# Kernel optimization log

Hardware: AMD Instinct MI355X
Metric: run time of the kernel (lower is better)

Reference implementation:

```python
import jax, jax.numpy as jnp
import numpy as np

IN_CH = 256
QK_CH = IN_CH // 8  # 32

def setup_inputs() -> dict:
    key = jax.random.key(0)
    ks = jax.random.split(key, 7)
    x = jax.random.normal(ks[0], (4, IN_CH, 64, 64), dtype=jnp.float32)
    s_in = 1.0 / np.sqrt(IN_CH)
    # 1x1 conv weights stored as [out_ch, in_ch]; biases [out_ch]
    Wq = jax.random.uniform(ks[1], (QK_CH, IN_CH), jnp.float32, -s_in, s_in)
    bq = jax.random.uniform(ks[2], (QK_CH,), jnp.float32, -s_in, s_in)
    Wk = jax.random.uniform(ks[3], (QK_CH, IN_CH), jnp.float32, -s_in, s_in)
    bk = jax.random.uniform(ks[4], (QK_CH,), jnp.float32, -s_in, s_in)
    Wv = jax.random.uniform(ks[5], (IN_CH, IN_CH), jnp.float32, -s_in, s_in)
    bv = jax.random.uniform(ks[6], (IN_CH,), jnp.float32, -s_in, s_in)
    return {"x": x, "Wq": Wq, "bq": bq, "Wk": Wk, "bk": bk, "Wv": Wv, "bv": bv}

def reference(x, Wq, bq, Wk, bk, Wv, bv):
    n, c, h, w = x.shape
    xf = x.reshape(n, c, h * w)  # [n, c, hw]
    # 1x1 convs == per-position channel matmuls
    q = jnp.einsum('oc,ncs->nos', Wq, xf) + bq[None, :, None]  # [n, c/8, hw]
    k = jnp.einsum('oc,ncs->nos', Wk, xf) + bk[None, :, None]  # [n, c/8, hw]
    v = jnp.einsum('oc,ncs->nos', Wv, xf) + bv[None, :, None]  # [n, c,  hw]
    # energy[n, i, j] = <q[:, i], k[:, j]>  (no scaling, as in original)
    energy = jnp.einsum('nci,ncj->nij', q, k)  # [n, hw, hw]
    attention = jax.nn.softmax(energy, axis=-1)
    # out[n, c, i] = sum_j v[n, c, j] * attention[n, i, j]
    out = jnp.einsum('ncj,nij->nci', v, attention)
    return out.reshape(n, c, h, w)
```

## Files before the change

### kernel.cpp

```cpp
#include <hip/hip_runtime.h>
#include <hip/hip_bf16.h>
#include <stdint.h>
#include <stddef.h>

typedef unsigned short u16;
typedef unsigned int   u32;
typedef __attribute__((ext_vector_type(8))) short bf16x8;
typedef __attribute__((ext_vector_type(4))) float f32x4;

#define LOG2E   1.44269504f
#define EXP_OFF 23.0831206f

static __device__ __forceinline__ float bf2f(u16 v) {
    u32 u = ((u32)v) << 16; float f; __builtin_memcpy(&f, &u, 4); return f;
}
static __device__ __forceinline__ u16 f2bf(float f) {
    u32 u; __builtin_memcpy(&u, &f, 4);
    u32 r = (u + 0x7fffu + ((u >> 16) & 1u)) >> 16; return (u16)r;
}
static __device__ __forceinline__ float as_f(u32 u) { float f; __builtin_memcpy(&f, &u, 4); return f; }
static __device__ __forceinline__ u32   as_u(float f) { u32 u; __builtin_memcpy(&u, &f, 4); return u; }

static __device__ __forceinline__ int detect_f32_wave0(const void* x, int t) {
    const u32* xw = (const u32*)x;
    int bad = 0;
    #pragma unroll
    for (int k = 0; k < 4; ++k) {
        u32 wv = xw[(t << 2) + k];
        int e = (wv >> 7) & 0xff;
        bad += (e >= 160);
    }
    unsigned long long m = __ballot(bad > 0);
    return (__popcll(m) >= 8) ? 1 : 0;
}


__global__ __launch_bounds__(256) void qkv_proj_mfma(
    const void* __restrict__ x,
    const void* __restrict__ Wq, const void* __restrict__ bq,
    const void* __restrict__ Wk, const void* __restrict__ bk,
    const void* __restrict__ Wv, const void* __restrict__ bv,
    u16* __restrict__ qws, u16* __restrict__ kws, u16* __restrict__ vws,
    int n_off, int nshiftp)
{
    __shared__ u16 Wl[64 * 256];
    __shared__ int dtf;

    const int t    = threadIdx.x;
    const int bid  = blockIdx.x;
    const int n_w  = bid & ((1 << nshiftp) - 1);
    const int rest = bid >> nshiftp;
    const int g    = rest % 5;
    const int it   = rest / 5;
    const int n_g  = n_off + n_w;
    const int i0   = it << 6;

    if (t < 64) { int f = detect_f32_wave0(x, t); if (t == 0) dtf = f; }
    __syncthreads();
    const bool isf32 = (dtf != 0);

    #pragma unroll
    for (int k = 0; k < 16; ++k) {
        int idx  = t + (k << 8);
        int row  = idx >> 6;
        int col4 = (idx & 63) << 2;
        const void* src; int srow;
        if (g == 0) {
            if (row < 32) { src = Wq; srow = row; }
            else          { src = Wk; srow = row - 32; }
        } else { src = Wv; srow = ((g - 1) << 6) + row; }
        ushort4 h;
        if (isf32) {
            float4 wv = *((const float4*)((const float*)src + srow * 256 + col4));
            h.x = f2bf(wv.x); h.y = f2bf(wv.y); h.z = f2bf(wv.z); h.w = f2bf(wv.w);
        } else {
            h = *((const ushort4*)((const u16*)src + srow * 256 + col4));
        }
        *(ushort4*)&Wl[(row << 8) + (col4 ^ ((row & 7) << 3))] = h;
    }
    __syncthreads();

    const int lane = t & 63;
    const int w    = t >> 6;
    const int n16  = lane & 15;
    const int quad = lane >> 4;
    const int i_b  = i0 + (w << 4);
    const int i    = i_b + n16;
    const int swz  = (n16 & 7) << 3;

    f32x4 acc[4];
    #pragma unroll
    for (int f = 0; f < 4; ++f) acc[f] = (f32x4){0.f, 0.f, 0.f, 0.f};

    if (isf32) {
        const float* xp = (const float*)x
            + (((size_t)(n_g * 256 + (quad << 3))) << 12) + i;
        float af[8];
        #pragma unroll
        for (int e = 0; e < 8; ++e) af[e] = xp[(size_t)e << 12];
        #pragma unroll
        for (int c8 = 0; c8 < 8; ++c8) {
            bf16x8 a;
            #pragma unroll
            for (int e = 0; e < 8; ++e) a[e] = (short)f2bf(af[e]);
            if (c8 < 7) {
                const float* xn = xp + (((size_t)(c8 + 1) << 5) << 12);
                #pragma unroll
                for (int e = 0; e < 8; ++e) af[e] = xn[(size_t)e << 12];
            }
            const int c0 = c8 << 5;
            #pragma unroll
            for (int f = 0; f < 4; ++f) {
                const int brow = (f << 4) + n16;
                bf16x8 b = *(const bf16x8*)
                    &Wl[(brow << 8) + ((c0 + (quad << 3)) ^ swz)];
                acc[f] = __builtin_amdgcn_mfma_f32_16x16x32_bf16(a, b, acc[f], 0, 0, 0);
            }
        }
    } else {
        const u16* xp = (const u16*)x
            + (((size_t)(n_g * 256 + (quad << 3))) << 12) + i;
        u16 af[8];
        #pragma unroll
        for (int e = 0; e < 8; ++e) af[e] = xp[(size_t)e << 12];
        #pragma unroll
        for (int c8 = 0; c8 < 8; ++c8) {
            bf16x8 a;
            #pragma unroll
            for (int e = 0; e < 8; ++e) a[e] = (short)af[e];
            if (c8 < 7) {
                const u16* xn = xp + (((size_t)(c8 + 1) << 5) << 12);
                #pragma unroll
                for (int e = 0; e < 8; ++e) af[e] = xn[(size_t)e << 12];
            }
            const int c0 = c8 << 5;
            #pragma unroll
            for (int f = 0; f < 4; ++f) {
                const int brow = (f << 4) + n16;
                bf16x8 b = *(const bf16x8*)
                    &Wl[(brow << 8) + ((c0 + (quad << 3)) ^ swz)];
                acc[f] = __builtin_amdgcn_mfma_f32_16x16x32_bf16(a, b, acc[f], 0, 0, 0);
            }
        }
    }

    if (g == 0) {
        #pragma unroll
        for (int f = 0; f < 4; ++f) {
            const int ol   = (f << 4) + n16;
            const bool isq = (ol < 32);
            const int och  = isq ? ol : (ol - 32);
            float bias;
            if (isf32) bias = ((const float*)(isq ? bq : bk))[och];
            else       bias = bf2f(((const u16*)(isq ? bq : bk))[och]);
            u16* dst = (isq ? qws : kws) + (((size_t)n_w) << 17) + och;
            const float scale = isq ? LOG2E : 1.0f;
            #pragma unroll
            for (int r = 0; r < 4; ++r) {
                const int ii = i_b + (quad << 2) + r;
                dst[(size_t)ii << 5] = f2bf((acc[f][r] + bias) * scale);
            }
        }
    } else {
        #pragma unroll
        for (int f = 0; f < 4; ++f) {
            const int c = ((g - 1) << 6) + (f << 4) + n16;
            float bias = isf32 ? ((const float*)bv)[c]
                               : bf2f(((const u16*)bv)[c]);
            const int i4 = i_b + (quad << 2);
            ushort4 h;
            h.x = f2bf(acc[f][0] + bias);
            h.y = f2bf(acc[f][1] + bias);
            h.z = f2bf(acc[f][2] + bias);
            h.w = f2bf(acc[f][3] + bias);
            const size_t addr = ((size_t)n_w << 20)
                + ((size_t)(c >> 4) << 16)
                + ((size_t)(i4 >> 5) << 9)
                + (size_t)((((((i4 & 31) >> 3) << 4) + (c & 15)) << 3) + (i4 & 7));
            *(ushort4*)(vws + addr) = h;
        }
    }
}

__global__ __launch_bounds__(1024) void flash_mfma9(
    const u16* __restrict__ qws, const u16* __restrict__ kws,
    const u16* __restrict__ vws, void* __restrict__ out,
    const void* __restrict__ x, int n_off, int nshift)
{
    __shared__ __align__(16) char arena[17920];
    __shared__ __align__(16) float lS[64];
    __shared__ int dtf;
    u16*   PsA  = (u16*)arena;
    float* Dbuf = (float*)arena;

    const int t    = threadIdx.x;
    const int lane = t & 63;
    const int w    = t >> 6;
    const int n16  = lane & 15;
    const int quad = lane >> 4;
    const int bid  = blockIdx.x;
    const int n_w  = bid & ((1 << nshift) - 1);
    const int qt   = bid >> nshift;
    const int n_g  = n_off + n_w;
    const int i0   = qt << 6;

    if (t < 64) {
        int f = detect_f32_wave0(x, t);
        if (t == 0) dtf = f;
        lS[t] = 0.f;
    }

    const u16* qb = qws + (((size_t)n_w) << 17);
    const u16* kb = kws + (((size_t)n_w) << 17);
    const u16* vb = vws + (((size_t)n_w) << 20);

    const int qsub_s = w & 3;
    const int jsub   = w >> 2;
    const int cq = w & 7;
    const int jq = w >> 3;

    const bf16x8 qfrag =
        *(const bf16x8*)(qb + ((size_t)(i0 + (qsub_s << 4) + n16) << 5) + (quad << 3));

    f32x4 acc[4][2];
    #pragma unroll
    for (int a = 0; a < 4; ++a)
        #pragma unroll
        for (int b = 0; b < 2; ++b) acc[a][b] = (f32x4){0.f, 0.f, 0.f, 0.f};
    float lp[4] = {0.f, 0.f, 0.f, 0.f};

    const int jcol = (jsub << 4) + n16;
    const int j8   = jcol >> 3;
    const int jlo  = jcol & 7;
    const int ksw  = (jq << 2) + quad;

    const u16* kp = kb + ((size_t)((jsub << 4) + n16) << 5) + (quad << 3);
    const u16* vfp0 = vb + ((size_t)(cq << 1) << 16) + ((size_t)jq << 9)
                         + ((size_t)((quad << 4) + n16) << 3);
    const u16* vfp1 = vfp0 + 65536;

    bf16x8 kcur, knext, vf0, vf1;

    kcur = *(const bf16x8*)(kp);
    {
        u16* Ps = PsA;
        const f32x4 z = {0.f, 0.f, 0.f, 0.f};
        f32x4 s = __builtin_amdgcn_mfma_f32_16x16x32_bf16(qfrag, kcur, z, 0, 0, 0);
        #pragma unroll
        for (int r = 0; r < 4; ++r) {
            const int qrow = (qsub_s << 4) + (quad << 2) + r;
            float p = exp2f(s[r] - EXP_OFF);
            u32 u = as_u(p) & 0xffff0000u;
            lp[r] += as_f(u);
            Ps[qrow * 64 + ((j8 ^ (qrow & 7)) << 3) + jlo] = (u16)(u >> 16);
        }
        knext = *(const bf16x8*)(kp + 2048);
        vf0 = *(const bf16x8*)(vfp0);
        vf1 = *(const bf16x8*)(vfp1);
    }
    __syncthreads();

    for (int tile = 1; tile < 64; ++tile) {
        const int par  = tile & 1;
        u16* Psc = PsA + (par << 12);
        u16* Psp = PsA + ((par ^ 1) << 12);

        kcur = knext;
        if (tile < 63) {
            knext = *(const bf16x8*)(kp + ((size_t)(tile + 1) << 11));
        }

        bf16x8 pa[4];
        #pragma unroll
        for (int qs = 0; qs < 4; ++qs) {
            const int qrow = (qs << 4) + n16;
            pa[qs] = *(const bf16x8*)&Psp[qrow * 64 + ((ksw ^ (qrow & 7)) << 3)];
        }
        #pragma unroll
        for (int qs = 0; qs < 4; ++qs) {
            acc[qs][0] = __builtin_amdgcn_mfma_f32_16x16x32_bf16(pa[qs], vf0, acc[qs][0], 0, 0, 0);
            acc[qs][1] = __builtin_amdgcn_mfma_f32_16x16x32_bf16(pa[qs], vf1, acc[qs][1], 0, 0, 0);
        }

        vf0 = *(const bf16x8*)(vfp0 + ((size_t)tile << 10));
        vf1 = *(const bf16x8*)(vfp1 + ((size_t)tile << 10));

        const f32x4 z = {0.f, 0.f, 0.f, 0.f};
        f32x4 s = __builtin_amdgcn_mfma_f32_16x16x32_bf16(qfrag, kcur, z, 0, 0, 0);
        #pragma unroll
        for (int r = 0; r < 4; ++r) {
            const int qrow = (qsub_s << 4) + (quad << 2) + r;
            float p = exp2f(s[r] - EXP_OFF);
            u32 u = as_u(p) & 0xffff0000u;
            lp[r] += as_f(u);
            Psc[qrow * 64 + ((j8 ^ (qrow & 7)) << 3) + jlo] = (u16)(u >> 16);
        }

        __syncthreads();
    }

    {
        u16* Psp = PsA + (1 << 12);
        bf16x8 pa[4];
        #pragma unroll
        for (int qs = 0; qs < 4; ++qs) {
            const int qrow = (qs << 4) + n16;
            pa[qs] = *(const bf16x8*)&Psp[qrow * 64 + ((ksw ^ (qrow & 7)) << 3)];
        }
        #pragma unroll
        for (int qs = 0; qs < 4; ++qs) {
            acc[qs][0] = __builtin_amdgcn_mfma_f32_16x16x32_bf16(pa[qs], vf0, acc[qs][0], 0, 0, 0);
            acc[qs][1] = __builtin_amdgcn_mfma_f32_16x16x32_bf16(pa[qs], vf1, acc[qs][1], 0, 0, 0);
        }
    }

    #pragma unroll
    for (int r = 0; r < 4; ++r) {
        lp[r] += __shfl_xor(lp[r], 1);
        lp[r] += __shfl_xor(lp[r], 2);
        lp[r] += __shfl_xor(lp[r], 4);
        lp[r] += __shfl_xor(lp[r], 8);
    }
    if (n16 == 0) {
        #pragma unroll
        for (int r = 0; r < 4; ++r)
            atomicAdd(&lS[(qsub_s << 4) + (quad << 2) + r], lp[r]);
    }
    __syncthreads();
    if (t < 64) lS[t] = 1.0f / lS[t];
    const bool isf32 = (dtf != 0);

    for (int chunk = 0; chunk < 4; ++chunk) {
        __syncthreads();
        if (jq == 1 && (cq >> 1) == chunk) {
            #pragma unroll
            for (int qs = 0; qs < 4; ++qs)
                #pragma unroll
                for (int cs = 0; cs < 2; ++cs)
                    *(f32x4*)&Dbuf[(((cq & 1) << 5) + (cs << 4) + n16) * 68 +
                                   (qs << 4) + (quad << 2)] = acc[qs][cs];
        }
        __syncthreads();
        if (jq == 0 && (cq >> 1) == chunk) {
            #pragma unroll
            for (int qs = 0; qs < 4; ++qs)
                #pragma unroll
                for (int cs = 0; cs < 2; ++cs) {
                    float* p = &Dbuf[(((cq & 1) << 5) + (cs << 4) + n16) * 68 +
                                     (qs << 4) + (quad << 2)];
                    f32x4 d = *(f32x4*)p;
                    d += acc[qs][cs];
                    *(f32x4*)p = d;
                }
        }
        __syncthreads();
        const int c_l = t >> 4;
        const int qg  = (t & 15) << 2;
        float4 d  = *(float4*)&Dbuf[c_l * 68 + qg];
        float4 rl = *(float4*)&lS[qg];
        const int c_glob = (chunk << 6) + c_l;
        const size_t ob = (((size_t)(n_g * 256 + c_glob)) << 12) + i0 + qg;
        if (isf32) {
            float4 o = make_float4(d.x * rl.x, d.y * rl.y, d.z * rl.z, d.w * rl.w);
            *(float4*)((float*)out + ob) = o;
        } else {
            union { uint2 v; u16 h[4]; } o;
            o.h[0] = f2bf(d.x * rl.x);
            o.h[1] = f2bf(d.y * rl.y);
            o.h[2] = f2bf(d.z * rl.z);
            o.h[3] = f2bf(d.w * rl.w);
            *(uint2*)((u16*)out + ob) = o.v;
        }
    }
}

extern "C" void kernel_launch(void* const* d_in, const int* in_sizes, int n_in,
                              void* d_out, int out_size, void* d_ws, size_t ws_size,
                              hipStream_t stream)
{
    const void* x  = d_in[0];
    const void* Wq = d_in[1];
    const void* bq = d_in[2];
    const void* Wk = d_in[3];
    const void* bk = d_in[4];
    const void* Wv = d_in[5];
    const void* bv = d_in[6];

    const size_t full_need = (size_t)(4u * 4096u) * (32 + 32 + 256) * 2;
    if (ws_size >= full_need) {
        u16* qws = (u16*)d_ws;
        u16* kws = qws + (size_t)4 * 4096 * 32;
        u16* vws = kws + (size_t)4 * 4096 * 32;
        qkv_proj_mfma<<<dim3(1280), dim3(256), 0, stream>>>(
            x, Wq, bq, Wk, bk, Wv, bv, qws, kws, vws, 0, 2);
        flash_mfma9<<<dim3(256), dim3(1024), 0, stream>>>(
            qws, kws, vws, d_out, x, 0, 2);
    } else {
        u16* qws = (u16*)d_ws;
        u16* kws = qws + (size_t)4096 * 32;
        u16* vws = kws + (size_t)4096 * 32;
        for (int n = 0; n < 4; ++n) {
            qkv_proj_mfma<<<dim3(320), dim3(256), 0, stream>>>(
                x, Wq, bq, Wk, bk, Wv, bv, qws, kws, vws, n, 0);
            flash_mfma9<<<dim3(64), dim3(1024), 0, stream>>>(
                qws, kws, vws, d_out, x, n, 0);
        }
    }
}
```

Baseline: 144.3 us.

## Process two key tiles per barrier with four-buffer P staging

```diff
diff --git a/kernel.cpp b/kernel.cpp
--- a/kernel.cpp
+++ b/kernel.cpp
@@ -182,15 +182,51 @@
     }
 }
 
-__global__ __launch_bounds__(1024) void flash_mfma9(
+static __device__ __forceinline__ void s_tile16(
+    const bf16x8 qfrag, const bf16x8 kc, char* __restrict__ PsW,
+    float* __restrict__ lp, const int* __restrict__ pwoff)
+{
+    const f32x4 zoff = {-EXP_OFF, -EXP_OFF, -EXP_OFF, -EXP_OFF};
+    f32x4 s = __builtin_amdgcn_mfma_f32_16x16x32_bf16(qfrag, kc, zoff, 0, 0, 0);
+    #pragma unroll
+    for (int r = 0; r < 4; ++r) {
+        float p = exp2f(s[r]);
+        u32 u = as_u(p) & 0xffff0000u;
+        lp[r] += as_f(u);
+        *(u16*)(PsW + pwoff[r]) = (u16)(u >> 16);
+    }
+}
+
+static __device__ __forceinline__ void pa_load(
+    const char* __restrict__ PsR, const int* __restrict__ paoff, bf16x8* pa)
+{
+    #pragma unroll
+    for (int qs = 0; qs < 4; ++qs)
+        pa[qs] = *(const bf16x8*)(PsR + paoff[qs]);
+}
+
+static __device__ __forceinline__ void pv_tile16(
+    const bf16x8* pa, const bf16x8 v0, const bf16x8 v1, f32x4 acc[4][2])
+{
+    #pragma unroll
+    for (int qs = 0; qs < 4; ++qs) {
+        acc[qs][0] = __builtin_amdgcn_mfma_f32_16x16x32_bf16(pa[qs], v0, acc[qs][0], 0, 0, 0);
+        acc[qs][1] = __builtin_amdgcn_mfma_f32_16x16x32_bf16(pa[qs], v1, acc[qs][1], 0, 0, 0);
+    }
+}
+
+__global__ __launch_bounds__(1024) void flash_mfma13(
     const u16* __restrict__ qws, const u16* __restrict__ kws,
     const u16* __restrict__ vws, void* __restrict__ out,
     const void* __restrict__ x, int n_off, int nshift)
 {
-    __shared__ __align__(16) char arena[17920];
+    __shared__ __align__(16) char arena[32768];
     __shared__ __align__(16) float lS[64];
     __shared__ int dtf;
-    u16*   PsA  = (u16*)arena;
+    char* buf0 = arena;
+    char* buf1 = arena + 8192;
+    char* buf2 = arena + 16384;
+    char* buf3 = arena + 24576;
     float* Dbuf = (float*)arena;
 
     const int t    = threadIdx.x;
@@ -234,84 +270,101 @@
     const int jlo  = jcol & 7;
     const int ksw  = (jq << 2) + quad;
 
+    int pwoff[4];
+    #pragma unroll
+    for (int r = 0; r < 4; ++r) {
+        const int qrow = (qsub_s << 4) + (quad << 2) + r;
+        pwoff[r] = (qrow * 64 + ((j8 ^ (qrow & 7)) << 3) + jlo) << 1;
+    }
+    int paoff[4];
+    #pragma unroll
+    for (int qs = 0; qs < 4; ++qs) {
+        const int qrow = (qs << 4) + n16;
+        paoff[qs] = (qrow * 64 + ((ksw ^ (qrow & 7)) << 3)) << 1;
+    }
+
     const u16* kp = kb + ((size_t)((jsub << 4) + n16) << 5) + (quad << 3);
     const u16* vfp0 = vb + ((size_t)(cq << 1) << 16) + ((size_t)jq << 9)
                          + ((size_t)((quad << 4) + n16) << 3);
     const u16* vfp1 = vfp0 + 65536;
 
-    bf16x8 kcur, knext, vf0, vf1;
-
-    kcur = *(const bf16x8*)(kp);
+    bf16x8 kc0, kc1, kn0, kn1;
+    bf16x8 vA0, vA1, vA2, vA3;
+    bf16x8 vB0, vB1, vB2, vB3;
+    bf16x8 pa[4];
+
+    kc0 = *(const bf16x8*)(kp);
+    kc1 = *(const bf16x8*)(kp + 2048);
+    s_tile16(qfrag, kc0, buf0, lp, pwoff);
+    s_tile16(qfrag, kc1, buf1, lp, pwoff);
+    kn0 = *(const bf16x8*)(kp + 2 * 2048);
+    kn1 = *(const bf16x8*)(kp + 3 * 2048);
+    vA0 = *(const bf16x8*)(vfp0);
+    vA1 = *(const bf16x8*)(vfp1);
+    vA2 = *(const bf16x8*)(vfp0 + 1024);
+    vA3 = *(const bf16x8*)(vfp1 + 1024);
+    __syncthreads();
+
+    const u16* kpp  = kp + 4 * 2048;
+    const u16* vpp0 = vfp0 + 2 * 1024;
+    const u16* vpp1 = vfp1 + 2 * 1024;
+
+    for (int pr = 0; pr < 15; ++pr) {
+        kc0 = kn0; kc1 = kn1;
+        kn0 = *(const bf16x8*)(kpp);
+        kn1 = *(const bf16x8*)(kpp + 2048);
+        kpp += 4096;
+        pa_load(buf0, paoff, pa);
+        s_tile16(qfrag, kc0, buf2, lp, pwoff);
+        pv_tile16(pa, vA0, vA1, acc);
+        pa_load(buf1, paoff, pa);
+        s_tile16(qfrag, kc1, buf3, lp, pwoff);
+        pv_tile16(pa, vA2, vA3, acc);
+        vB0 = *(const bf16x8*)(vpp0);
+        vB1 = *(const bf16x8*)(vpp1);
+        vB2 = *(const bf16x8*)(vpp0 + 1024);
+        vB3 = *(const bf16x8*)(vpp1 + 1024);
+        vpp0 += 2048; vpp1 += 2048;
+        __syncthreads();
+
+        kc0 = kn0; kc1 = kn1;
+        kn0 = *(const bf16x8*)(kpp);
+        kn1 = *(const bf16x8*)(kpp + 2048);
+        kpp += 4096;
+        pa_load(buf2, paoff, pa);
+        s_tile16(qfrag, kc0, buf0, lp, pwoff);
+        pv_tile16(pa, vB0, vB1, acc);
+        pa_load(buf3, paoff, pa);
+        s_tile16(qfrag, kc1, buf1, lp, pwoff);
+        pv_tile16(pa, vB2, vB3, acc);
+        vA0 = *(const bf16x8*)(vpp0);
+        vA1 = *(const bf16x8*)(vpp1);
+        vA2 = *(const bf16x8*)(vpp0 + 1024);
+        vA3 = *(const bf16x8*)(vpp1 + 1024);
+        vpp0 += 2048; vpp1 += 2048;
+        __syncthreads();
+    }
+
     {
-        u16* Ps = PsA;
-        const f32x4 z = {0.f, 0.f, 0.f, 0.f};
-        f32x4 s = __builtin_amdgcn_mfma_f32_16x16x32_bf16(qfrag, kcur, z, 0, 0, 0);
-        #pragma unroll
-        for (int r = 0; r < 4; ++r) {
-            const int qrow = (qsub_s << 4) + (quad << 2) + r;
-            float p = exp2f(s[r] - EXP_OFF);
-            u32 u = as_u(p) & 0xffff0000u;
-            lp[r] += as_f(u);
-            Ps[qrow * 64 + ((j8 ^ (qrow & 7)) << 3) + jlo] = (u16)(u >> 16);
-        }
-        knext = *(const bf16x8*)(kp + 2048);
-        vf0 = *(const bf16x8*)(vfp0);
-        vf1 = *(const bf16x8*)(vfp1);
-    }
-    __syncthreads();
-
-    for (int tile = 1; tile < 64; ++tile) {
-        const int par  = tile & 1;
-        u16* Psc = PsA + (par << 12);
-        u16* Psp = PsA + ((par ^ 1) << 12);
-
-        kcur = knext;
-        if (tile < 63) {
-            knext = *(const bf16x8*)(kp + ((size_t)(tile + 1) << 11));
-        }
-
-        bf16x8 pa[4];
-        #pragma unroll
-        for (int qs = 0; qs < 4; ++qs) {
-            const int qrow = (qs << 4) + n16;
-            pa[qs] = *(const bf16x8*)&Psp[qrow * 64 + ((ksw ^ (qrow & 7)) << 3)];
-        }
-        #pragma unroll
-        for (int qs = 0; qs < 4; ++qs) {
-            acc[qs][0] = __builtin_amdgcn_mfma_f32_16x16x32_bf16(pa[qs], vf0, acc[qs][0], 0, 0, 0);
-            acc[qs][1] = __builtin_amdgcn_mfma_f32_16x16x32_bf16(pa[qs], vf1, acc[qs][1], 0, 0, 0);
-        }
-
-        vf0 = *(const bf16x8*)(vfp0 + ((size_t)tile << 10));
-        vf1 = *(const bf16x8*)(vfp1 + ((size_t)tile << 10));
-
-        const f32x4 z = {0.f, 0.f, 0.f, 0.f};
-        f32x4 s = __builtin_amdgcn_mfma_f32_16x16x32_bf16(qfrag, kcur, z, 0, 0, 0);
-        #pragma unroll
-        for (int r = 0; r < 4; ++r) {
-            const int qrow = (qsub_s << 4) + (quad << 2) + r;
-            float p = exp2f(s[r] - EXP_OFF);
-            u32 u = as_u(p) & 0xffff0000u;
-            lp[r] += as_f(u);
-            Psc[qrow * 64 + ((j8 ^ (qrow & 7)) << 3) + jlo] = (u16)(u >> 16);
-        }
-
+        kc0 = kn0; kc1 = kn1;
+        pa_load(buf0, paoff, pa);
+        s_tile16(qfrag, kc0, buf2, lp, pwoff);
+        pv_tile16(pa, vA0, vA1, acc);
+        pa_load(buf1, paoff, pa);
+        s_tile16(qfrag, kc1, buf3, lp, pwoff);
+        pv_tile16(pa, vA2, vA3, acc);
+        vB0 = *(const bf16x8*)(vpp0);
+        vB1 = *(const bf16x8*)(vpp1);
+        vB2 = *(const bf16x8*)(vpp0 + 1024);
+        vB3 = *(const bf16x8*)(vpp1 + 1024);
         __syncthreads();
     }
 
     {
-        u16* Psp = PsA + (1 << 12);
-        bf16x8 pa[4];
-        #pragma unroll
-        for (int qs = 0; qs < 4; ++qs) {
-            const int qrow = (qs << 4) + n16;
-            pa[qs] = *(const bf16x8*)&Psp[qrow * 64 + ((ksw ^ (qrow & 7)) << 3)];
-        }
-        #pragma unroll
-        for (int qs = 0; qs < 4; ++qs) {
-            acc[qs][0] = __builtin_amdgcn_mfma_f32_16x16x32_bf16(pa[qs], vf0, acc[qs][0], 0, 0, 0);
-            acc[qs][1] = __builtin_amdgcn_mfma_f32_16x16x32_bf16(pa[qs], vf1, acc[qs][1], 0, 0, 0);
-        }
+        pa_load(buf2, paoff, pa);
+        pv_tile16(pa, vB0, vB1, acc);
+        pa_load(buf3, paoff, pa);
+        pv_tile16(pa, vB2, vB3, acc);
     }
 
     #pragma unroll
@@ -393,7 +446,7 @@
         u16* vws = kws + (size_t)4 * 4096 * 32;
         qkv_proj_mfma<<<dim3(1280), dim3(256), 0, stream>>>(
             x, Wq, bq, Wk, bk, Wv, bv, qws, kws, vws, 0, 2);
-        flash_mfma9<<<dim3(256), dim3(1024), 0, stream>>>(
+        flash_mfma13<<<dim3(256), dim3(1024), 0, stream>>>(
             qws, kws, vws, d_out, x, 0, 2);
     } else {
         u16* qws = (u16*)d_ws;
@@ -402,7 +455,7 @@
         for (int n = 0; n < 4; ++n) {
             qkv_proj_mfma<<<dim3(320), dim3(256), 0, stream>>>(
                 x, Wq, bq, Wk, bk, Wv, bv, qws, kws, vws, n, 0);
-            flash_mfma9<<<dim3(64), dim3(1024), 0, stream>>>(
+            flash_mfma13<<<dim3(64), dim3(1024), 0, stream>>>(
                 qws, kws, vws, d_out, x, n, 0);
         }
     }
```

Result: no change. 145.1 us (+0.6%).
